# Performance work log

Measured on AMD Instinct MI355X. Metric: run time of the kernel, lower is better.

The kernel has to match this reference:

```python
import jax, jax.numpy as jnp
import numpy as np

N_NODES = 30000
N_REL = 200
N_EDGES = 150000
N_EDGES_NHOP = 30000
NFEAT = 100
NHID = 100
REL_DIM = 100
NHEADS = 2
ALPHA = 0.2  # leaky relu slope


def setup_inputs() -> dict:
    key = jax.random.key(0)
    ks = jax.random.split(key, 16)
    s = 0.1
    D = NHEADS * NHID
    inp = {}
    inp["entity_embeddings"] = jax.random.normal(ks[0], (N_NODES, NFEAT), jnp.float32)
    inp["relation_embed"] = jax.random.normal(ks[1], (N_REL, REL_DIM), jnp.float32)
    inp["edge_list"] = jax.random.randint(ks[2], (2, N_EDGES), 0, N_NODES)
    inp["edge_type"] = jax.random.randint(ks[3], (N_EDGES,), 0, N_REL)
    inp["edge_embed"] = jax.random.normal(ks[4], (N_EDGES, REL_DIM), jnp.float32)
    inp["edge_list_nhop"] = jax.random.randint(ks[5], (2, N_EDGES_NHOP), 0, N_NODES)
    inp["edge_type_nhop"] = jax.random.randint(ks[6], (N_EDGES_NHOP, 2), 0, N_REL)
    inp["entity_embeddings_mapping"] = jax.random.normal(ks[7], (N_NODES, NFEAT), jnp.float32)
    # learned params (xavier-like scale)
    inp["a_heads"] = jax.random.normal(ks[8], (NHEADS, NHID, 2 * NFEAT + REL_DIM), jnp.float32) * s
    inp["a2_heads"] = jax.random.normal(ks[9], (NHEADS, NHID), jnp.float32) * s
    inp["W"] = jax.random.normal(ks[10], (REL_DIM, D), jnp.float32) * s
    inp["a_out"] = jax.random.normal(ks[11], (D, 3 * D), jnp.float32) * s
    inp["a2_out"] = jax.random.normal(ks[12], (D,), jnp.float32) * s
    return inp


def _att_layer(x, src, dst, edge_embed, a, a2, n_nodes, concat):
    # Sparse graph attention (KBGAT style). a: [out, 2*in + rel_dim].
    in_dim = x.shape[1]
    a_src, a_dst, a_rel = a[:, :in_dim], a[:, in_dim:2 * in_dim], a[:, 2 * in_dim:]
    # edge_m = a @ cat(x[src], x[dst], edge_embed)^T, computed without the big concat
    edge_m = x[src] @ a_src.T + x[dst] @ a_dst.T + edge_embed @ a_rel.T  # [E, out]
    powers = -jax.nn.leaky_relu(edge_m @ a2, ALPHA)                      # [E]
    edge_e = jnp.exp(powers)                                             # [E]
    e_rowsum = jax.ops.segment_sum(edge_e, src, num_segments=n_nodes)    # [N]
    e_rowsum = jnp.where(e_rowsum == 0.0, 1e-12, e_rowsum)
    h = jax.ops.segment_sum(edge_e[:, None] * edge_m, src, num_segments=n_nodes)  # [N, out]
    h = h / e_rowsum[:, None]
    return jax.nn.elu(h) if concat else h


def reference(entity_embeddings, relation_embed, edge_list, edge_type, edge_embed,
              edge_list_nhop, edge_type_nhop, entity_embeddings_mapping,
              a_heads, a2_heads, W, a_out, a2_out):
    N = entity_embeddings.shape[0]
    src = jnp.concatenate([edge_list[0], edge_list_nhop[0]])
    dst = jnp.concatenate([edge_list[1], edge_list_nhop[1]])
    # 2-hop edge embedding = sum of the two relation embeddings on the path
    ee_nhop = relation_embed[edge_type_nhop[:, 0]] + relation_embed[edge_type_nhop[:, 1]]
    ee1 = jnp.concatenate([edge_embed, ee_nhop], axis=0)
    h1 = _att_layer(entity_embeddings, src, dst, ee1, a_heads[0], a2_heads[0], N, True)
    h2 = _att_layer(entity_embeddings, src, dst, ee1, a_heads[1], a2_heads[1], N, True)
    h = jnp.concatenate([h1, h2], axis=1)  # [N, 2*nhid]; dropout p=0 (eval)
    out_relation = relation_embed @ W      # [R, 2*nhid]
    ee2 = jnp.concatenate([out_relation[edge_type],
                           out_relation[edge_type_nhop[:, 0]] + out_relation[edge_type_nhop[:, 1]]],
                          axis=0)
    out_entity = _att_layer(h, src, dst, ee2, a_out, a2_out, N, False)
    return jax.nn.elu(out_entity), out_relation
```

## Files before the change

kernel.cpp:

```cpp
#include <hip/hip_runtime.h>

#define N_NODES 30000
#define E1 150000
#define EN 30000
#define ET 180000
#define LALPHA 0.2f
#define NB_SCAN 118

typedef unsigned int u32;
typedef unsigned short u16;
typedef __attribute__((ext_vector_type(8))) short short8;
typedef __attribute__((ext_vector_type(4))) short short4v;
typedef __attribute__((ext_vector_type(4))) float f32x4;

__device__ __forceinline__ float bf2f(u16 u){ return __uint_as_float(((u32)u)<<16); }
__device__ __forceinline__ float2 bfp2(u32 u){
  return make_float2(__uint_as_float(u<<16), __uint_as_float(u & 0xffff0000u));
}
__device__ __forceinline__ u16 f2bf(float f){
  u32 x = __float_as_uint(f);
  return (u16)((x + 0x7fffu + ((x>>16)&1u)) >> 16);
}
__device__ __forceinline__ u32 pk(float x, float y){
  return ((u32)f2bf(x)) | (((u32)f2bf(y))<<16);
}
__device__ __forceinline__ float wredf(float v){
  #pragma unroll
  for(int o=32;o>0;o>>=1) v += __shfl_xor(v, o, 64);
  return v;
}
__device__ __forceinline__ float eluf(float y){ return (y>0.f)? y : expm1f(y); }
__device__ __forceinline__ float ld1(const void* p, int i, int f){
  return f ? ((const float*)p)[i] : bf2f(((const u16*)p)[i]);
}
__device__ __forceinline__ float2 ldp(const void* p, int i, int f){
  if(f){ return ((const float2*)p)[i]; }
  return bfp2(((const u32*)p)[i]);
}
__device__ __forceinline__ void st1(void* p, int i, float v, int f){
  if(f) ((float*)p)[i] = v; else ((u16*)p)[i] = f2bf(v);
}

__device__ __forceinline__ short8 frag_zero(){
  short8 r;
  #pragma unroll
  for(int i=0;i<8;i++) r[i]=0;
  return r;
}
__device__ __forceinline__ short8 ldfragb(const u16* p, int idx){
  short8 r;
  short4v lo = *(const short4v*)(p+idx);
  short4v hi = *(const short4v*)(p+idx+4);
  #pragma unroll
  for(int i=0;i<4;i++){ r[i]=lo[i]; r[4+i]=hi[i]; }
  return r;
}
__device__ __forceinline__ short8 ldfragb_p4(const u16* p, int idx){
  short8 r=frag_zero();
  short4v lo = *(const short4v*)(p+idx);
  #pragma unroll
  for(int i=0;i<4;i++) r[i]=lo[i];
  return r;
}

__global__ void k_detect(const u32* x, int* flag){
  int t = threadIdx.x;
  int c = 0;
  #pragma unroll
  for(int i=0;i<4;i++){
    u32 v = x[t*4+i];
    u32 lo = v & 0xffffu;
    u32 e = (lo>>7)&0xffu;
    c += (lo==0u || (e>=100u && e<=140u)) ? 1 : 0;
  }
  __shared__ int sd[256];
  sd[t]=c; __syncthreads();
  for(int o=128;o>0;o>>=1){ if(t<o) sd[t]+=sd[t+o]; __syncthreads(); }
  if(t==0) *flag = (sd[0] > 512) ? 0 : 1;
}

__global__ void k_prep(const void* ent, const void* ah, const void* ao,
                       u16* entB, u16* ahB, u16* aoB, const int* flag){
  int f = *flag;
  int gid = blockIdx.x*256 + threadIdx.x;
  int stride = gridDim.x*256;
  const int T0=750000, T1=765000, T2=795000;
  for(int i=gid; i<T2; i+=stride){
    const void* src; u16* dst; int g;
    if(i<T0){ src=ent; dst=entB; g=i; }
    else if(i<T1){ src=ah; dst=ahB; g=i-T0; }
    else { src=ao; dst=aoB; g=i-T1; }
    if(f){
      float4 v = ((const float4*)src)[g];
      int base=g*4;
      dst[base]=f2bf(v.x); dst[base+1]=f2bf(v.y); dst[base+2]=f2bf(v.z); dst[base+3]=f2bf(v.w);
    } else {
      ((short4v*)dst)[g] = ((const short4v*)src)[g];
    }
  }
}

__global__ void k_outrel(const void* rel, const void* W, float* outrel, void* out, const int* flag){
  int f = *flag;
  int t = blockIdx.x*blockDim.x + threadIdx.x;
  if(t >= 200*200) return;
  int r = t / 200, j = t - r*200;
  float acc = 0.f;
  for(int k=0;k<100;k++) acc += ld1(rel, r*100+k, f) * ld1(W, k*200+j, f);
  outrel[t] = acc;
  st1(out, 6000000 + t, acc, f);
}

__global__ void k_small_b(const void* ah, const void* a2h, const void* ao, const void* a2o,
                          float* b1, float* b2, const int* flag){
  int f = *flag;
  int i = blockIdx.x*4 + (threadIdx.x>>6);
  int L = threadIdx.x & 63;
  if(i >= 1200) return;
  float a = 0.f;
  if(i < 600){
    int hd = i/300, k = i - hd*300;
    for(int j=L; j<100; j+=64)
      a += ld1(a2h, hd*100+j, f) * ld1(ah, hd*30000 + j*300 + k, f);
    a = wredf(a);
    if(L==0) b1[i] = a;
  } else {
    int k = i - 600;
    for(int j=L; j<200; j+=64)
      a += ld1(a2o, j, f) * ld1(ao, j*600 + k, f);
    a = wredf(a);
    if(L==0) b2[k] = a;
  }
}

__global__ void k_small_c(const void* rel, const float* outrel, const float* b1, const float* b2,
                          float* c1, float* c2, const int* flag){
  int f = *flag;
  int i = blockIdx.x*4 + (threadIdx.x>>6);
  int L = threadIdx.x & 63;
  if(i >= 600) return;
  float a = 0.f;
  if(i < 400){
    int hd = i/200, r = i - hd*200;
    for(int k=L; k<100; k+=64)
      a += b1[hd*300+200+k] * ld1(rel, r*100+k, f);
    a = wredf(a);
    if(L==0) c1[i] = a;
  } else {
    int r = i - 400;
    for(int k=L; k<200; k+=64)
      a += b2[400+k] * outrel[r*200+k];
    a = wredf(a);
    if(L==0) c2[r] = a;
  }
}

__global__ void k_count(const int* src1, const int* srcN, int* cnt){
  int e = blockIdx.x*256 + threadIdx.x;
  if(e>=ET) return;
  int s = (e<E1)? src1[e] : srcN[e-E1];
  atomicAdd(&cnt[s],1);
}

__global__ void k_scan1(const int* cnt, int* ofs, int* bsum){
  __shared__ int sd[256];
  int b=blockIdx.x, t=threadIdx.x;
  int idx=b*256+t;
  int v=(idx<N_NODES)? cnt[idx] : 0;
  sd[t]=v; __syncthreads();
  for(int o=1;o<256;o<<=1){
    int u=(t>=o)? sd[t-o]:0;
    __syncthreads();
    sd[t]+=u; __syncthreads();
  }
  if(idx<N_NODES) ofs[idx]=sd[t]-v;
  if(t==255) bsum[b]=sd[255];
}

__global__ void k_scan2(const int* bsum, int* bstart, int* ofs){
  __shared__ int sd[128];
  int t=threadIdx.x;
  int v=(t<NB_SCAN)? bsum[t]:0;
  sd[t]=v; __syncthreads();
  for(int o=1;o<128;o<<=1){
    int u=(t>=o)? sd[t-o]:0;
    __syncthreads();
    sd[t]+=u; __syncthreads();
  }
  if(t<NB_SCAN) bstart[t]=sd[t]-v;
  if(t==127) ofs[N_NODES]=sd[127];
}

__global__ void k_scan3(int* ofs, int* cur, const int* bstart){
  int b=blockIdx.x, t=threadIdx.x;
  int idx=b*256+t;
  if(idx>=N_NODES) return;
  int v = ofs[idx] + bstart[b];
  ofs[idx]=v; cur[idx]=v;
}

__global__ void k_scatter(const int* src1, const int* srcN, int* cur, int* eord){
  int e = blockIdx.x*256 + threadIdx.x;
  if(e>=ET) return;
  int s = (e<E1)? src1[e] : srcN[e-E1];
  int p = atomicAdd(&cur[s],1);
  eord[p]=e;
}

__global__ void k_q1(const void* ent, const float* b1, float* q1, const int* flag){
  int f = *flag;
  int n = blockIdx.x*4 + (threadIdx.x>>6);
  if(n>=N_NODES) return;
  int L = threadIdx.x & 63;
  float d00=0,d01=0,d10=0,d11=0;
  if(L<50){
    float2 xv = ldp(ent, n*50+L, f);
    int k0=2*L;
    d00 = xv.x*b1[k0]     + xv.y*b1[k0+1];
    d01 = xv.x*b1[100+k0] + xv.y*b1[100+k0+1];
    d10 = xv.x*b1[300+k0] + xv.y*b1[300+k0+1];
    d11 = xv.x*b1[400+k0] + xv.y*b1[400+k0+1];
  }
  d00=wredf(d00); d01=wredf(d01); d10=wredf(d10); d11=wredf(d11);
  if(L==0){ q1[n*4+0]=d00; q1[n*4+1]=d01; q1[n*4+2]=d10; q1[n*4+3]=d11; }
}

__global__ void k_edge1(const void* ee, const int* etn,
                        const int* src1,const int* dst1,const int* srcN,const int* dstN,
                        const float* b1, const float* c1, const float* q1, float* w1, const int* flag){
  int f = *flag;
  int e = blockIdx.x*4 + (threadIdx.x>>6);
  if(e>=ET) return;
  int L = threadIdx.x & 63;
  float r0, r1;
  if(e<E1){
    float p0=0,p1=0;
    if(L<50){ float2 ev = ldp(ee, e*50+L, f); int k0=2*L;
      p0 = ev.x*b1[200+k0]+ev.y*b1[200+k0+1];
      p1 = ev.x*b1[500+k0]+ev.y*b1[500+k0+1]; }
    r0 = wredf(p0); r1 = wredf(p1);
  } else {
    int en = e-E1;
    int t0 = etn[en*2], t1 = etn[en*2+1];
    r0 = c1[t0]+c1[t1];
    r1 = c1[200+t0]+c1[200+t1];
  }
  if(L==0){
    int s,d;
    if(e<E1){ s=src1[e]; d=dst1[e]; } else { int en=e-E1; s=srcN[en]; d=dstN[en]; }
    float p0 = q1[s*4+0] + q1[d*4+1] + r0;
    float p1 = q1[s*4+2] + q1[d*4+3] + r1;
    p0 = (p0>=0.f)? p0 : LALPHA*p0;
    p1 = (p1>=0.f)? p1 : LALPHA*p1;
    w1[e]    = expf(-p0);
    w1[ET+e] = expf(-p1);
  }
}

__global__ void k_acc1(const int* ofs, const int* eord,
                       const int* dst1, const int* dstN, const int* etn,
                       const void* ent, const void* ee, const void* rel,
                       const float* w1, u32* Gq, float* rs1, const int* flag){
  int f = *flag;
  int n = blockIdx.x*4 + (threadIdx.x>>6);
  if(n>=N_NODES) return;
  int L = threadIdx.x & 63;
  int beg = ofs[n], end = ofs[n+1];
  float av0x=0,av0y=0,av1x=0,av1y=0, aw0x=0,aw0y=0,aw1x=0,aw1y=0;
  float r0=0, r1=0;
  for(int i=beg;i<end;i++){
    int e = eord[i];
    float w0 = w1[e], wh = w1[ET+e];
    r0 += w0; r1 += wh;
    bool orig = e<E1;
    int en = e-E1;
    int d = orig? dst1[e] : dstN[en];
    if(L<50){
      float2 xv = ldp(ent, d*50+L, f);
      av0x += w0*xv.x; av0y += w0*xv.y;
      av1x += wh*xv.x; av1y += wh*xv.y;
      float2 ev;
      if(orig){ ev = ldp(ee, e*50+L, f); }
      else { int t0=etn[en*2], t1=etn[en*2+1];
             float2 e0=ldp(rel, t0*50+L, f), e1=ldp(rel, t1*50+L, f);
             ev = make_float2(e0.x+e1.x, e0.y+e1.y); }
      aw0x += w0*ev.x; aw0y += w0*ev.y;
      aw1x += wh*ev.x; aw1y += wh*ev.y;
    }
  }
  float i0 = (r0==0.f)? 0.f : 1.f/r0;
  float i1 = (r1==0.f)? 0.f : 1.f/r1;
  if(L<50){
    u32* g0 = Gq + n*100;
    u32* g1 = Gq + 3000000 + n*100;
    g0[L]    = pk(av0x*i0, av0y*i0);
    g0[50+L] = pk(aw0x*i0, aw0y*i0);
    g1[L]    = pk(av1x*i1, av1y*i1);
    g1[50+L] = pk(aw1x*i1, aw1y*i1);
  }
  if(L==0){ rs1[n]=r0; rs1[N_NODES+n]=r1; }
}

__global__ __launch_bounds__(256) void k_gemm1m(const u16* G, const u16* ahB, const u16* entB,
                        const float* rs1, u16* h){
  int hd = blockIdx.y;
  int wid = threadIdx.x>>6, l = threadIdx.x&63;
  int lr = l&15, lg = l>>4;
  int m0 = blockIdx.x*32;
  int row0 = m0 + lr, row1 = m0 + 16 + lr;
  bool hi_ok = (m0+16) < N_NODES;
  const u16* Gh0 = G + hd*6000000 + row0*200;
  const u16* Gh1 = G + hd*6000000 + row1*200;
  const u16* A = ahB + hd*30000;
  f32x4 acc[2][2];
  #pragma unroll
  for(int mi=0;mi<2;mi++)
    #pragma unroll
    for(int ntl=0;ntl<2;ntl++) acc[mi][ntl]=(f32x4){0.f,0.f,0.f,0.f};
  #pragma unroll
  for(int k0=0;k0<100;k0+=32){
    int kb = k0 + lg*8;
    short8 a0 = (kb+8<=100)? ldfragb(entB, row0*100+kb)
              : (kb<100    ? ldfragb_p4(entB, row0*100+kb) : frag_zero());
    short8 a1 = frag_zero();
    if(hi_ok){
      if(kb+8<=100) a1 = ldfragb(entB, row1*100+kb);
      else if(kb<100) a1 = ldfragb_p4(entB, row1*100+kb);
    }
    #pragma unroll
    for(int ntl=0;ntl<2;ntl++){
      int j = (ntl*4+wid)*16 + lr;
      short8 b = frag_zero();
      if(j<100){
        if(kb+8<=100) b = ldfragb(A, j*300 + kb);
        else if(kb<100) b = ldfragb_p4(A, j*300 + kb);
      }
      acc[0][ntl] = __builtin_amdgcn_mfma_f32_16x16x32_bf16(a0, b, acc[0][ntl], 0,0,0);
      acc[1][ntl] = __builtin_amdgcn_mfma_f32_16x16x32_bf16(a1, b, acc[1][ntl], 0,0,0);
    }
  }
  #pragma unroll
  for(int k0=0;k0<200;k0+=32){
    int kb = k0 + lg*8;
    short8 a0 = (kb+8<=200)? ldfragb(Gh0, kb) : frag_zero();
    short8 a1 = (hi_ok && kb+8<=200)? ldfragb(Gh1, kb) : frag_zero();
    #pragma unroll
    for(int ntl=0;ntl<2;ntl++){
      int j = (ntl*4+wid)*16 + lr;
      short8 b = (j<100 && kb+8<=200)? ldfragb(A, j*300 + 100 + kb) : frag_zero();
      acc[0][ntl] = __builtin_amdgcn_mfma_f32_16x16x32_bf16(a0, b, acc[0][ntl], 0,0,0);
      acc[1][ntl] = __builtin_amdgcn_mfma_f32_16x16x32_bf16(a1, b, acc[1][ntl], 0,0,0);
    }
  }
  #pragma unroll
  for(int mi=0;mi<2;mi++){
    if(mi==1 && !hi_ok) break;
    #pragma unroll
    for(int r=0;r<4;r++){
      int rr = m0 + mi*16 + lg*4 + r;
      float sc = (rs1[hd*N_NODES+rr]==0.f)? 0.f : 1.f;
      #pragma unroll
      for(int ntl=0;ntl<2;ntl++){
        int j = (ntl*4+wid)*16 + lr;
        if(j<100) h[rr*200 + hd*100 + j] = f2bf(eluf(acc[mi][ntl][r]*sc));
      }
    }
  }
}

__global__ void k_q2(const u32* h32, const float* b2, float* q2){
  int n = blockIdx.x*4 + (threadIdx.x>>6);
  if(n>=N_NODES) return;
  int L = threadIdx.x&63;
  float ds=0, dd=0;
  if(L<50){
    float2 a = bfp2(h32[n*100+2*L]);
    float2 b = bfp2(h32[n*100+2*L+1]);
    int k0=4*L;
    ds = a.x*b2[k0]+a.y*b2[k0+1]+b.x*b2[k0+2]+b.y*b2[k0+3];
    dd = a.x*b2[200+k0]+a.y*b2[200+k0+1]+b.x*b2[200+k0+2]+b.y*b2[200+k0+3];
  }
  ds=wredf(ds); dd=wredf(dd);
  if(L==0){ q2[n*2]=ds; q2[n*2+1]=dd; }
}

__global__ void k_edge2(const int* src1,const int* dst1,const int* srcN,const int* dstN,
                        const int* et, const int* etn, const float* c2, const float* q2, float* w2){
  int e = blockIdx.x*256+threadIdx.x;
  if(e>=ET) return;
  int s,d; float r;
  if(e<E1){ s=src1[e]; d=dst1[e]; r = c2[et[e]]; }
  else { int en=e-E1; s=srcN[en]; d=dstN[en]; r = c2[etn[en*2]]+c2[etn[en*2+1]]; }
  float p = q2[s*2] + q2[d*2+1] + r;
  p = (p>=0.f)? p : LALPHA*p;
  w2[e] = expf(-p);
}

__global__ void k_acc2(const int* ofs, const int* eord,
                       const int* dst1,const int* dstN, const int* et,const int* etn,
                       const u32* h32, const float4* or4, const float* w2,
                       u32* Gq, float* rs2){
  int n = blockIdx.x*4 + (threadIdx.x>>6);
  if(n>=N_NODES) return;
  int L = threadIdx.x&63;
  int beg=ofs[n], end=ofs[n+1];
  float rv=0;
  float avx=0,avy=0,avz=0,avw=0, awx=0,awy=0,awz=0,aww=0;
  for(int i=beg;i<end;i++){
    int e=eord[i];
    float w=w2[e];
    rv += w;
    bool orig = e<E1; int en=e-E1;
    int d = orig? dst1[e]:dstN[en];
    if(L<50){
      float2 ha = bfp2(h32[d*100+2*L]);
      float2 hb = bfp2(h32[d*100+2*L+1]);
      avx+=w*ha.x; avy+=w*ha.y; avz+=w*hb.x; avw+=w*hb.y;
      float ex,ey,ez,ew;
      if(orig){ float4 o=or4[et[e]*50+L]; ex=o.x;ey=o.y;ez=o.z;ew=o.w; }
      else { float4 a=or4[etn[en*2]*50+L], b=or4[etn[en*2+1]*50+L];
             ex=a.x+b.x; ey=a.y+b.y; ez=a.z+b.z; ew=a.w+b.w; }
      awx+=w*ex; awy+=w*ey; awz+=w*ez; aww+=w*ew;
    }
  }
  float inv = (rv==0.f)? 0.f : 1.f/rv;
  if(L<50){
    u32* g = Gq + n*200;
    g[2*L]       = pk(avx*inv, avy*inv);
    g[2*L+1]     = pk(avz*inv, avw*inv);
    g[100+2*L]   = pk(awx*inv, awy*inv);
    g[100+2*L+1] = pk(awz*inv, aww*inv);
  }
  if(L==0) rs2[n]=rv;
}

__global__ __launch_bounds__(256) void k_gemm2m(const u16* G, const u16* aoB, const u16* h,
                        const float* rs2, void* out, const int* flag){
  int f = *flag;
  int wid = threadIdx.x>>6, l = threadIdx.x&63;
  int lr = l&15, lg = l>>4;
  int m0 = blockIdx.x*32;
  int row0 = m0 + lr, row1 = m0 + 16 + lr;
  bool hi_ok = (m0+16) < N_NODES;
  const u16* h0 = h + row0*200;
  const u16* h1 = h + row1*200;
  const u16* g0 = G + row0*400;
  const u16* g1 = G + row1*400;
  f32x4 acc[2][4];
  #pragma unroll
  for(int mi=0;mi<2;mi++)
    #pragma unroll
    for(int ntl=0;ntl<4;ntl++) acc[mi][ntl]=(f32x4){0.f,0.f,0.f,0.f};
  #pragma unroll
  for(int k0=0;k0<200;k0+=32){
    int kb = k0 + lg*8;
    short8 a0 = (kb+8<=200)? ldfragb(h0, kb) : frag_zero();
    short8 a1 = (hi_ok && kb+8<=200)? ldfragb(h1, kb) : frag_zero();
    #pragma unroll
    for(int ntl=0;ntl<4;ntl++){
      int j = (ntl*4+wid)*16 + lr;
      short8 b = (j<200 && kb+8<=200)? ldfragb(aoB, j*600 + kb) : frag_zero();
      acc[0][ntl] = __builtin_amdgcn_mfma_f32_16x16x32_bf16(a0, b, acc[0][ntl], 0,0,0);
      acc[1][ntl] = __builtin_amdgcn_mfma_f32_16x16x32_bf16(a1, b, acc[1][ntl], 0,0,0);
    }
  }
  #pragma unroll
  for(int k0=0;k0<400;k0+=32){
    int kb = k0 + lg*8;
    short8 a0 = (kb+8<=400)? ldfragb(g0, kb) : frag_zero();
    short8 a1 = (hi_ok && kb+8<=400)? ldfragb(g1, kb) : frag_zero();
    #pragma unroll
    for(int ntl=0;ntl<4;ntl++){
      int j = (ntl*4+wid)*16 + lr;
      short8 b = (j<200 && kb+8<=400)? ldfragb(aoB, j*600 + 200 + kb) : frag_zero();
      acc[0][ntl] = __builtin_amdgcn_mfma_f32_16x16x32_bf16(a0, b, acc[0][ntl], 0,0,0);
      acc[1][ntl] = __builtin_amdgcn_mfma_f32_16x16x32_bf16(a1, b, acc[1][ntl], 0,0,0);
    }
  }
  #pragma unroll
  for(int mi=0;mi<2;mi++){
    if(mi==1 && !hi_ok) break;
    #pragma unroll
    for(int r=0;r<4;r++){
      int rr = m0 + mi*16 + lg*4 + r;
      float sc = (rs2[rr]==0.f)? 0.f : 1.f;
      #pragma unroll
      for(int ntl=0;ntl<4;ntl++){
        int j = (ntl*4+wid)*16 + lr;
        if(j<200) st1(out, rr*200 + j, eluf(acc[mi][ntl][r]*sc), f);
      }
    }
  }
}

extern "C" void kernel_launch(void* const* d_in, const int* in_sizes, int n_in,
                              void* d_out, int out_size, void* d_ws, size_t ws_size,
                              hipStream_t stream) {
  const void* ent = d_in[0];
  const void* rel = d_in[1];
  const int* el  = (const int*)d_in[2];
  const int* et  = (const int*)d_in[3];
  const void* ee  = d_in[4];
  const int* eln = (const int*)d_in[5];
  const int* etn = (const int*)d_in[6];
  const void* ah  = d_in[8];
  const void* a2h = d_in[9];
  const void* W   = d_in[10];
  const void* ao  = d_in[11];
  const void* a2o = d_in[12];

  float* wsf    = (float*)d_ws;
  int*   flag   = (int*)wsf;
  float* outrel = wsf+4;
  float* b1     = wsf+40008;
  float* b2     = wsf+40608;
  float* c1     = wsf+41208;
  float* c2     = wsf+41608;
  float* q1     = wsf+41808;
  float* q2     = wsf+161808;
  float* w1     = wsf+221808;
  float* w2     = wsf+581808;
  float* rs1    = wsf+761808;
  float* rs2    = wsf+821808;
  int*   ofs    = (int*)(wsf+851808);
  int*   cnt    = ofs+30001;
  int*   cur    = cnt+30000;
  int*   eord   = cur+30000;
  int*   bsum   = (int*)(wsf+1121812);
  int*   bstart = bsum+128;
  u16*   G      = (u16*)(wsf+1122072);
  u16*   h      = (u16*)(wsf+7122072);
  h             = (u16*)(wsf+7122072);
  u16*   entB   = (u16*)(wsf+10122072);
  u16*   ahB    = (u16*)(wsf+11622072);
  u16*   aoB    = (u16*)(wsf+11652072);

  const int* src1 = el;
  const int* dst1 = el + E1;
  const int* srcN = eln;
  const int* dstN = eln + EN;

  k_detect<<<1,256,0,stream>>>((const u32*)ent, flag);
  hipMemsetAsync(cnt, 0, 30000*sizeof(int), stream);
  k_prep<<<1024,256,0,stream>>>(ent, ah, ao, entB, ahB, aoB, flag);
  k_small_b<<<300,256,0,stream>>>(ah,a2h,ao,a2o,b1,b2,flag);
  k_outrel<<<(200*200+255)/256,256,0,stream>>>(rel, W, outrel, d_out, flag);
  k_small_c<<<150,256,0,stream>>>(rel, outrel, b1, b2, c1, c2, flag);
  k_count<<<(ET+255)/256,256,0,stream>>>(src1, srcN, cnt);
  k_scan1<<<NB_SCAN,256,0,stream>>>(cnt, ofs, bsum);
  k_scan2<<<1,128,0,stream>>>(bsum, bstart, ofs);
  k_scan3<<<NB_SCAN,256,0,stream>>>(ofs, cur, bstart);
  k_scatter<<<(ET+255)/256,256,0,stream>>>(src1, srcN, cur, eord);
  k_q1<<<(N_NODES+3)/4,256,0,stream>>>(ent, b1, q1, flag);
  k_edge1<<<(ET+3)/4,256,0,stream>>>(ee, etn, src1, dst1, srcN, dstN, b1, c1, q1, w1, flag);
  k_acc1<<<(N_NODES+3)/4,256,0,stream>>>(ofs, eord, dst1, dstN, etn,
                                         ent, ee, rel, w1, (u32*)G, rs1, flag);
  dim3 g1grid((N_NODES+31)/32, 2);
  k_gemm1m<<<g1grid,256,0,stream>>>(G, ahB, entB, rs1, h);
  k_q2<<<(N_NODES+3)/4,256,0,stream>>>((const u32*)h, b2, q2);
  k_edge2<<<(ET+255)/256,256,0,stream>>>(src1, dst1, srcN, dstN, et, etn, c2, q2, w2);
  k_acc2<<<(N_NODES+3)/4,256,0,stream>>>(ofs, eord, dst1, dstN, et, etn,
                                         (const u32*)h, (const float4*)outrel, w2, (u32*)G, rs2);
  k_gemm2m<<<(N_NODES+31)/32,256,0,stream>>>(G, aoB, h, rs2, d_out, flag);
}
```

Before: 294.3 us.

## Split edge1 into thread-per-edge smem-staged kernel and nhop kernel; read bf16 entity copy

The original edge-score kernel, which spent one 64-lane wave per edge, is split in two. Original edges get a kernel where each block stages 256 edge-embedding rows in padded shared memory, then each thread computes its edge's two dot products serially. N-hop edges get a simple thread-per-edge kernel. k_q1 and k_acc1 now read the precomputed bf16 entity copy instead of the flag-dependent input, which cuts load bandwidth and branching. The cost is a large shared-memory footprint per block (about 54KB) that limits occupancy, plus a serial 50-step loop per thread.

```diff
diff --git a/kernel.cpp b/kernel.cpp
--- a/kernel.cpp
+++ b/kernel.cpp
@@ -207,14 +207,13 @@
   eord[p]=e;
 }
 
-__global__ void k_q1(const void* ent, const float* b1, float* q1, const int* flag){
-  int f = *flag;
+__global__ void k_q1(const u32* entB2, const float* b1, float* q1){
   int n = blockIdx.x*4 + (threadIdx.x>>6);
   if(n>=N_NODES) return;
   int L = threadIdx.x & 63;
   float d00=0,d01=0,d10=0,d11=0;
   if(L<50){
-    float2 xv = ldp(ent, n*50+L, f);
+    float2 xv = bfp2(entB2[n*50+L]);
     int k0=2*L;
     d00 = xv.x*b1[k0]     + xv.y*b1[k0+1];
     d01 = xv.x*b1[100+k0] + xv.y*b1[100+k0+1];
@@ -225,41 +224,60 @@
   if(L==0){ q1[n*4+0]=d00; q1[n*4+1]=d01; q1[n*4+2]=d10; q1[n*4+3]=d11; }
 }
 
-__global__ void k_edge1(const void* ee, const int* etn,
-                        const int* src1,const int* dst1,const int* srcN,const int* dstN,
-                        const float* b1, const float* c1, const float* q1, float* w1, const int* flag){
-  int f = *flag;
-  int e = blockIdx.x*4 + (threadIdx.x>>6);
-  if(e>=ET) return;
-  int L = threadIdx.x & 63;
-  float r0, r1;
-  if(e<E1){
-    float p0=0,p1=0;
-    if(L<50){ float2 ev = ldp(ee, e*50+L, f); int k0=2*L;
-      p0 = ev.x*b1[200+k0]+ev.y*b1[200+k0+1];
-      p1 = ev.x*b1[500+k0]+ev.y*b1[500+k0+1]; }
-    r0 = wredf(p0); r1 = wredf(p1);
-  } else {
-    int en = e-E1;
-    int t0 = etn[en*2], t1 = etn[en*2+1];
-    r0 = c1[t0]+c1[t1];
-    r1 = c1[200+t0]+c1[200+t1];
-  }
-  if(L==0){
-    int s,d;
-    if(e<E1){ s=src1[e]; d=dst1[e]; } else { int en=e-E1; s=srcN[en]; d=dstN[en]; }
-    float p0 = q1[s*4+0] + q1[d*4+1] + r0;
-    float p1 = q1[s*4+2] + q1[d*4+3] + r1;
-    p0 = (p0>=0.f)? p0 : LALPHA*p0;
-    p1 = (p1>=0.f)? p1 : LALPHA*p1;
-    w1[e]    = expf(-p0);
-    w1[ET+e] = expf(-p1);
-  }
+__global__ __launch_bounds__(256) void k_edge1a(const void* ee,
+    const int* src1, const int* dst1, const float* b1, const float* q1,
+    float* w1, const int* flag){
+  int f = *flag;
+  __shared__ u32 sd[256*53];
+  __shared__ float bb[200];
+  int t = threadIdx.x;
+  int e0 = blockIdx.x*256;
+  if(t<100){ bb[t]=b1[200+t]; bb[100+t]=b1[500+t]; }
+  int nr = E1 - e0; if(nr>256) nr=256;
+  int tot = nr*50;
+  for(int i=t; i<tot; i+=256){
+    int r = i/50, j = i - r*50;
+    float2 v = ldp(ee, e0*50 + i, f);
+    sd[r*53 + j] = pk(v.x, v.y);
+  }
+  __syncthreads();
+  int e = e0 + t;
+  if(e >= E1 || t >= nr) return;
+  float r0=0.f, r1=0.f;
+  #pragma unroll 5
+  for(int k=0;k<50;k++){
+    float2 v = bfp2(sd[t*53+k]);
+    r0 += v.x*bb[2*k]     + v.y*bb[2*k+1];
+    r1 += v.x*bb[100+2*k] + v.y*bb[100+2*k+1];
+  }
+  int s=src1[e], d=dst1[e];
+  float p0 = q1[s*4+0] + q1[d*4+1] + r0;
+  float p1 = q1[s*4+2] + q1[d*4+3] + r1;
+  p0 = (p0>=0.f)? p0 : LALPHA*p0;
+  p1 = (p1>=0.f)? p1 : LALPHA*p1;
+  w1[e]    = expf(-p0);
+  w1[ET+e] = expf(-p1);
+}
+
+__global__ void k_edge1b(const int* etn, const int* srcN, const int* dstN,
+                         const float* c1, const float* q1, float* w1){
+  int en = blockIdx.x*256+threadIdx.x;
+  if(en>=EN) return;
+  int t0=etn[en*2], t1=etn[en*2+1];
+  float r0 = c1[t0]+c1[t1];
+  float r1 = c1[200+t0]+c1[200+t1];
+  int s=srcN[en], d=dstN[en];
+  float p0 = q1[s*4+0]+q1[d*4+1]+r0;
+  float p1 = q1[s*4+2]+q1[d*4+3]+r1;
+  p0=(p0>=0.f)?p0:LALPHA*p0;
+  p1=(p1>=0.f)?p1:LALPHA*p1;
+  w1[E1+en]    = expf(-p0);
+  w1[ET+E1+en] = expf(-p1);
 }
 
 __global__ void k_acc1(const int* ofs, const int* eord,
                        const int* dst1, const int* dstN, const int* etn,
-                       const void* ent, const void* ee, const void* rel,
+                       const u32* entB2, const void* ee, const void* rel,
                        const float* w1, u32* Gq, float* rs1, const int* flag){
   int f = *flag;
   int n = blockIdx.x*4 + (threadIdx.x>>6);
@@ -276,7 +294,7 @@
     int en = e-E1;
     int d = orig? dst1[e] : dstN[en];
     if(L<50){
-      float2 xv = ldp(ent, d*50+L, f);
+      float2 xv = bfp2(entB2[d*50+L]);
       av0x += w0*xv.x; av0y += w0*xv.y;
       av1x += wh*xv.x; av1y += wh*xv.y;
       float2 ev;
@@ -530,7 +548,6 @@
   int*   bstart = bsum+128;
   u16*   G      = (u16*)(wsf+1122072);
   u16*   h      = (u16*)(wsf+7122072);
-  h             = (u16*)(wsf+7122072);
   u16*   entB   = (u16*)(wsf+10122072);
   u16*   ahB    = (u16*)(wsf+11622072);
   u16*   aoB    = (u16*)(wsf+11652072);
@@ -551,10 +568,11 @@
   k_scan2<<<1,128,0,stream>>>(bsum, bstart, ofs);
   k_scan3<<<NB_SCAN,256,0,stream>>>(ofs, cur, bstart);
   k_scatter<<<(ET+255)/256,256,0,stream>>>(src1, srcN, cur, eord);
-  k_q1<<<(N_NODES+3)/4,256,0,stream>>>(ent, b1, q1, flag);
-  k_edge1<<<(ET+3)/4,256,0,stream>>>(ee, etn, src1, dst1, srcN, dstN, b1, c1, q1, w1, flag);
+  k_q1<<<(N_NODES+3)/4,256,0,stream>>>((const u32*)entB, b1, q1);
+  k_edge1a<<<(E1+255)/256,256,0,stream>>>(ee, src1, dst1, b1, q1, w1, flag);
+  k_edge1b<<<(EN+255)/256,256,0,stream>>>(etn, srcN, dstN, c1, q1, w1);
   k_acc1<<<(N_NODES+3)/4,256,0,stream>>>(ofs, eord, dst1, dstN, etn,
-                                         ent, ee, rel, w1, (u32*)G, rs1, flag);
+                                         (const u32*)entB, ee, rel, w1, (u32*)G, rs1, flag);
   dim3 g1grid((N_NODES+31)/32, 2);
   k_gemm1m<<<g1grid,256,0,stream>>>(G, ahB, entB, rs1, h);
   k_q2<<<(N_NODES+3)/4,256,0,stream>>>((const u32*)h, b2, q2);
```

Result: no change. 297.8 us (+1.2%).
